# Optimization experiments

Hardware: AMD Instinct MI355X
Metric: run time of the kernel (lower is better)

Reference implementation:

```python
import jax, jax.numpy as jnp
import numpy as np

FEATURE_DIM = 32

def setup_inputs() -> dict:
    key = jax.random.key(0)
    k_pts, k_w1, k_b1, k_w2, k_b2 = jax.random.split(key, 5)
    B, N = 4096, 4096
    points = jax.random.normal(k_pts, (B, N, 2), dtype=jnp.float32)
    # torch Linear default init: U(-1/sqrt(fan_in), 1/sqrt(fan_in))
    lim1 = 1.0 / np.sqrt(10.0)
    lim2 = 1.0 / np.sqrt(64.0)
    W1 = jax.random.uniform(k_w1, (10, 64), minval=-lim1, maxval=lim1, dtype=jnp.float32)
    b1 = jax.random.uniform(k_b1, (64,), minval=-lim1, maxval=lim1, dtype=jnp.float32)
    W2 = jax.random.uniform(k_w2, (64, FEATURE_DIM), minval=-lim2, maxval=lim2, dtype=jnp.float32)
    b2 = jax.random.uniform(k_b2, (FEATURE_DIM,), minval=-lim2, maxval=lim2, dtype=jnp.float32)
    return {"points": points, "W1": W1, "b1": b1, "W2": W2, "b2": b2}

def _geo_features(points):
    # points: (B, N, 2) -> (B, 10)
    bbox_min = jnp.min(points, axis=1)            # (B, 2)
    bbox_max = jnp.max(points, axis=1)            # (B, 2)
    bbox_center = (bbox_min + bbox_max) * 0.5
    bbox_size = bbox_max - bbox_min
    centroid = jnp.mean(points, axis=1)           # (B, 2)
    std = jnp.std(points, axis=1)                 # population std (ddof=0), matches np.std
    diffs = points - centroid[:, None, :]         # (B, N, 2)
    distances = jnp.linalg.norm(diffs, axis=2)    # (B, N)
    dist_mean = jnp.mean(distances, axis=1)       # (B,)
    dist_std = jnp.std(distances, axis=1)         # (B,)
    return jnp.concatenate(
        [bbox_center, bbox_size, centroid, std, dist_mean[:, None], dist_std[:, None]],
        axis=1,
    )  # (B, 10)

def reference(points, W1, b1, W2, b2):
    geo = _geo_features(points)                   # (B, 10)
    h = jax.nn.relu(geo @ W1 + b1)                # (B, 64)
    return jax.nn.relu(h @ W2 + b2)               # (B, feature_dim)
```

## Files before the change

### kernel.cpp

```cpp
#include <hip/hip_runtime.h>
#include <math.h>

#define NPTS 4096
#define BLOCK 256
#define PTS4 (NPTS / 2)
#define ITERS (PTS4 / BLOCK)

__global__ __launch_bounds__(BLOCK, 4) void geo_mlp_kernel(
    const float* __restrict__ points,
    const float* __restrict__ W1,
    const float* __restrict__ b1,
    const float* __restrict__ W2,
    const float* __restrict__ b2,
    float* __restrict__ out)
{
    __shared__ float4 pts[PTS4];
    __shared__ float wred[4][9];
    __shared__ float h[64];

    const int tid  = threadIdx.x;
    const int lane = tid & 63;
    const int wave = tid >> 6;
    const int b    = blockIdx.x;

    float w1r[10];
    float w2r[32];
    float b1r = 0.f, b2r = 0.f;
    const int col   = lane & 31;
    const int rbase = (lane >> 5) * 32;
    if (wave == 0) {
        #pragma unroll
        for (int i = 0; i < 10; ++i)
            w1r[i] = W1[i * 64 + lane];
        b1r = b1[lane];
        #pragma unroll
        for (int r = 0; r < 32; ++r)
            w2r[r] = W2[(rbase + r) * 32 + col];
        b2r = (lane < 32) ? b2[col] : 0.0f;
    }

    const float4* __restrict__ src =
        (const float4*)(points + (size_t)b * NPTS * 2);

    float minx =  INFINITY, miny =  INFINITY;
    float maxx = -INFINITY, maxy = -INFINITY;
    float sx = 0.f, sy = 0.f, sxx = 0.f, syy = 0.f;

    #pragma unroll
    for (int i = 0; i < ITERS; ++i) {
        const int idx = tid + i * BLOCK;
        float4 v = src[idx];
        pts[idx] = v;
        minx = fminf(minx, fminf(v.x, v.z));
        maxx = fmaxf(maxx, fmaxf(v.x, v.z));
        miny = fminf(miny, fminf(v.y, v.w));
        maxy = fmaxf(maxy, fmaxf(v.y, v.w));
        sx += v.x + v.z;
        sy += v.y + v.w;
        sxx = fmaf(v.x, v.x, sxx); sxx = fmaf(v.z, v.z, sxx);
        syy = fmaf(v.y, v.y, syy); syy = fmaf(v.w, v.w, syy);
    }

    #pragma unroll
    for (int off = 32; off > 0; off >>= 1) {
        minx = fminf(minx, __shfl_down(minx, off));
        maxx = fmaxf(maxx, __shfl_down(maxx, off));
        miny = fminf(miny, __shfl_down(miny, off));
        maxy = fmaxf(maxy, __shfl_down(maxy, off));
        sx  += __shfl_down(sx,  off);
        sy  += __shfl_down(sy,  off);
        sxx += __shfl_down(sxx, off);
        syy += __shfl_down(syy, off);
    }
    if (lane == 0) {
        wred[wave][0] = minx; wred[wave][1] = maxx;
        wred[wave][2] = miny; wred[wave][3] = maxy;
        wred[wave][4] = sx;   wred[wave][5] = sy;
        wred[wave][6] = sxx;  wred[wave][7] = syy;
    }
    __syncthreads();

    const float invN = 1.0f / (float)NPTS;
    const float cx = ((wred[0][4] + wred[1][4]) + (wred[2][4] + wred[3][4])) * invN;
    const float cy = ((wred[0][5] + wred[1][5]) + (wred[2][5] + wred[3][5])) * invN;

    float sd = 0.f;
    #pragma unroll
    for (int i = 0; i < ITERS; ++i) {
        float4 v = pts[tid + i * BLOCK];
        float dx0 = v.x - cx, dy0 = v.y - cy;
        float dx1 = v.z - cx, dy1 = v.w - cy;
        sd += sqrtf(fmaf(dx0, dx0, dy0 * dy0));
        sd += sqrtf(fmaf(dx1, dx1, dy1 * dy1));
    }
    #pragma unroll
    for (int off = 32; off > 0; off >>= 1)
        sd += __shfl_down(sd, off);
    if (lane == 0)
        wred[wave][8] = sd;
    __syncthreads();

    if (wave == 0) {
        float fminx = fminf(fminf(wred[0][0], wred[1][0]), fminf(wred[2][0], wred[3][0]));
        float fmaxx = fmaxf(fmaxf(wred[0][1], wred[1][1]), fmaxf(wred[2][1], wred[3][1]));
        float fminy = fminf(fminf(wred[0][2], wred[1][2]), fminf(wred[2][2], wred[3][2]));
        float fmaxy = fmaxf(fmaxf(wred[0][3], wred[1][3]), fmaxf(wred[2][3], wred[3][3]));
        float fsxx = (wred[0][6] + wred[1][6]) + (wred[2][6] + wred[3][6]);
        float fsyy = (wred[0][7] + wred[1][7]) + (wred[2][7] + wred[3][7]);
        float fsd  = (wred[0][8] + wred[1][8]) + (wred[2][8] + wred[3][8]);

        float dist_mean = fsd * invN;
        float ed2 = (fsxx + fsyy) * invN - (cx * cx + cy * cy);
        float dist_std  = sqrtf(fmaxf(ed2 - dist_mean * dist_mean, 0.f));
        float stdx = sqrtf(fmaxf(fsxx * invN - cx * cx, 0.f));
        float stdy = sqrtf(fmaxf(fsyy * invN - cy * cy, 0.f));

        float g[10];
        g[0] = (fminx + fmaxx) * 0.5f;
        g[1] = (fminy + fmaxy) * 0.5f;
        g[2] = fmaxx - fminx;
        g[3] = fmaxy - fminy;
        g[4] = cx;
        g[5] = cy;
        g[6] = stdx;
        g[7] = stdy;
        g[8] = dist_mean;
        g[9] = dist_std;

        float acc = b1r;
        #pragma unroll
        for (int i = 0; i < 10; ++i)
            acc = fmaf(g[i], w1r[i], acc);
        h[lane] = fmaxf(acc, 0.f);

        asm volatile("s_waitcnt lgkmcnt(0)" ::: "memory");

        float acc2 = b2r;
        #pragma unroll
        for (int r = 0; r < 32; ++r)
            acc2 = fmaf(h[rbase + r], w2r[r], acc2);
        acc2 += __shfl_down(acc2, 32);
        if (lane < 32)
            out[(size_t)b * 32 + lane] = fmaxf(acc2, 0.f);
    }
}

extern "C" void kernel_launch(void* const* d_in, const int* in_sizes, int n_in,
                              void* d_out, int out_size, void* d_ws, size_t ws_size,
                              hipStream_t stream) {
    const float* points = (const float*)d_in[0];
    const float* W1     = (const float*)d_in[1];
    const float* b1     = (const float*)d_in[2];
    const float* W2     = (const float*)d_in[3];
    const float* b2     = (const float*)d_in[4];
    float* out          = (float*)d_out;

    const int B = in_sizes[0] / (NPTS * 2);
    geo_mlp_kernel<<<B, BLOCK, 0, stream>>>(points, W1, b1, W2, b2, out);
}
```

Measured before the change: 28.77 us.

## Process eight batches per block with register-prefetched software pipeline

Each block now handles eight batch rows. The next row's global loads are issued into registers while the current row's distance pass and MLP run. This is meant to hide global-load latency and spread the cost of weight loads and launch across rows. In exchange the grid shrinks to B/8 blocks, register pressure rises from the prefetch buffer, and a row count not divisible by eight would be handled incorrectly.

```diff
diff --git a/kernel.cpp b/kernel.cpp
--- a/kernel.cpp
+++ b/kernel.cpp
@@ -5,6 +5,7 @@
 #define BLOCK 256
 #define PTS4 (NPTS / 2)
 #define ITERS (PTS4 / BLOCK)
+#define BPB 8
 
 __global__ __launch_bounds__(BLOCK, 4) void geo_mlp_kernel(
     const float* __restrict__ points,
@@ -15,13 +16,13 @@
     float* __restrict__ out)
 {
     __shared__ float4 pts[PTS4];
-    __shared__ float wred[4][9];
+    __shared__ float wred[2][4][9];
     __shared__ float h[64];
 
     const int tid  = threadIdx.x;
     const int lane = tid & 63;
     const int wave = tid >> 6;
-    const int b    = blockIdx.x;
+    const size_t b0 = (size_t)blockIdx.x * BPB;
 
     float w1r[10];
     float w2r[32];
@@ -39,109 +40,137 @@
         b2r = (lane < 32) ? b2[col] : 0.0f;
     }
 
-    const float4* __restrict__ src =
-        (const float4*)(points + (size_t)b * NPTS * 2);
+    const float invN = 1.0f / (float)NPTS;
+    float4 pn[ITERS];
 
-    float minx =  INFINITY, miny =  INFINITY;
-    float maxx = -INFINITY, maxy = -INFINITY;
-    float sx = 0.f, sy = 0.f, sxx = 0.f, syy = 0.f;
+    auto issue_loads = [&](int j) {
+        const float4* __restrict__ src =
+            (const float4*)(points + (b0 + (size_t)j) * NPTS * 2);
+        #pragma unroll
+        for (int i = 0; i < ITERS; ++i)
+            pn[i] = src[tid + i * BLOCK];
+    };
 
-    #pragma unroll
-    for (int i = 0; i < ITERS; ++i) {
-        const int idx = tid + i * BLOCK;
-        float4 v = src[idx];
-        pts[idx] = v;
-        minx = fminf(minx, fminf(v.x, v.z));
-        maxx = fmaxf(maxx, fmaxf(v.x, v.z));
-        miny = fminf(miny, fminf(v.y, v.w));
-        maxy = fmaxf(maxy, fmaxf(v.y, v.w));
-        sx += v.x + v.z;
-        sy += v.y + v.w;
-        sxx = fmaf(v.x, v.x, sxx); sxx = fmaf(v.z, v.z, sxx);
-        syy = fmaf(v.y, v.y, syy); syy = fmaf(v.w, v.w, syy);
-    }
+    auto stage = [&](int par) {
+        float minx =  INFINITY, miny =  INFINITY;
+        float maxx = -INFINITY, maxy = -INFINITY;
+        float sx = 0.f, sy = 0.f, sxx = 0.f, syy = 0.f;
+        #pragma unroll
+        for (int i = 0; i < ITERS; ++i) {
+            float4 v = pn[i];
+            pts[tid + i * BLOCK] = v;
+            minx = fminf(minx, fminf(v.x, v.z));
+            maxx = fmaxf(maxx, fmaxf(v.x, v.z));
+            miny = fminf(miny, fminf(v.y, v.w));
+            maxy = fmaxf(maxy, fmaxf(v.y, v.w));
+            sx += v.x + v.z;
+            sy += v.y + v.w;
+            sxx = fmaf(v.x, v.x, sxx); sxx = fmaf(v.z, v.z, sxx);
+            syy = fmaf(v.y, v.y, syy); syy = fmaf(v.w, v.w, syy);
+        }
+        #pragma unroll
+        for (int off = 32; off > 0; off >>= 1) {
+            minx = fminf(minx, __shfl_down(minx, off));
+            maxx = fmaxf(maxx, __shfl_down(maxx, off));
+            miny = fminf(miny, __shfl_down(miny, off));
+            maxy = fmaxf(maxy, __shfl_down(maxy, off));
+            sx  += __shfl_down(sx,  off);
+            sy  += __shfl_down(sy,  off);
+            sxx += __shfl_down(sxx, off);
+            syy += __shfl_down(syy, off);
+        }
+        if (lane == 0) {
+            wred[par][wave][0] = minx; wred[par][wave][1] = maxx;
+            wred[par][wave][2] = miny; wred[par][wave][3] = maxy;
+            wred[par][wave][4] = sx;   wred[par][wave][5] = sy;
+            wred[par][wave][6] = sxx;  wred[par][wave][7] = syy;
+        }
+    };
 
-    #pragma unroll
-    for (int off = 32; off > 0; off >>= 1) {
-        minx = fminf(minx, __shfl_down(minx, off));
-        maxx = fmaxf(maxx, __shfl_down(maxx, off));
-        miny = fminf(miny, __shfl_down(miny, off));
-        maxy = fmaxf(maxy, __shfl_down(maxy, off));
-        sx  += __shfl_down(sx,  off);
-        sy  += __shfl_down(sy,  off);
-        sxx += __shfl_down(sxx, off);
-        syy += __shfl_down(syy, off);
-    }
-    if (lane == 0) {
-        wred[wave][0] = minx; wred[wave][1] = maxx;
-        wred[wave][2] = miny; wred[wave][3] = maxy;
-        wred[wave][4] = sx;   wred[wave][5] = sy;
-        wred[wave][6] = sxx;  wred[wave][7] = syy;
-    }
+    issue_loads(0);
+    stage(0);
+    if (BPB > 1) issue_loads(1);
     __syncthreads();
 
-    const float invN = 1.0f / (float)NPTS;
-    const float cx = ((wred[0][4] + wred[1][4]) + (wred[2][4] + wred[3][4])) * invN;
-    const float cy = ((wred[0][5] + wred[1][5]) + (wred[2][5] + wred[3][5])) * invN;
+    for (int j = 0; j < BPB; ++j) {
+        const int par = j & 1;
+        const float cx = ((wred[par][0][4] + wred[par][1][4]) +
+                          (wred[par][2][4] + wred[par][3][4])) * invN;
+        const float cy = ((wred[par][0][5] + wred[par][1][5]) +
+                          (wred[par][2][5] + wred[par][3][5])) * invN;
 
-    float sd = 0.f;
-    #pragma unroll
-    for (int i = 0; i < ITERS; ++i) {
-        float4 v = pts[tid + i * BLOCK];
-        float dx0 = v.x - cx, dy0 = v.y - cy;
-        float dx1 = v.z - cx, dy1 = v.w - cy;
-        sd += sqrtf(fmaf(dx0, dx0, dy0 * dy0));
-        sd += sqrtf(fmaf(dx1, dx1, dy1 * dy1));
-    }
-    #pragma unroll
-    for (int off = 32; off > 0; off >>= 1)
-        sd += __shfl_down(sd, off);
-    if (lane == 0)
-        wred[wave][8] = sd;
-    __syncthreads();
+        float sd = 0.f;
+        #pragma unroll
+        for (int i = 0; i < ITERS; ++i) {
+            float4 v = pts[tid + i * BLOCK];
+            float dx0 = v.x - cx, dy0 = v.y - cy;
+            float dx1 = v.z - cx, dy1 = v.w - cy;
+            sd += sqrtf(fmaf(dx0, dx0, dy0 * dy0));
+            sd += sqrtf(fmaf(dx1, dx1, dy1 * dy1));
+        }
+        #pragma unroll
+        for (int off = 32; off > 0; off >>= 1)
+            sd += __shfl_down(sd, off);
+        if (lane == 0)
+            wred[par][wave][8] = sd;
+        __syncthreads();
 
-    if (wave == 0) {
-        float fminx = fminf(fminf(wred[0][0], wred[1][0]), fminf(wred[2][0], wred[3][0]));
-        float fmaxx = fmaxf(fmaxf(wred[0][1], wred[1][1]), fmaxf(wred[2][1], wred[3][1]));
-        float fminy = fminf(fminf(wred[0][2], wred[1][2]), fminf(wred[2][2], wred[3][2]));
-        float fmaxy = fmaxf(fmaxf(wred[0][3], wred[1][3]), fmaxf(wred[2][3], wred[3][3]));
-        float fsxx = (wred[0][6] + wred[1][6]) + (wred[2][6] + wred[3][6]);
-        float fsyy = (wred[0][7] + wred[1][7]) + (wred[2][7] + wred[3][7]);
-        float fsd  = (wred[0][8] + wred[1][8]) + (wred[2][8] + wred[3][8]);
+        if (j + 1 < BPB) {
+            stage((j + 1) & 1);
+            if (j + 2 < BPB) issue_loads(j + 2);
+        }
 
-        float dist_mean = fsd * invN;
-        float ed2 = (fsxx + fsyy) * invN - (cx * cx + cy * cy);
-        float dist_std  = sqrtf(fmaxf(ed2 - dist_mean * dist_mean, 0.f));
-        float stdx = sqrtf(fmaxf(fsxx * invN - cx * cx, 0.f));
-        float stdy = sqrtf(fmaxf(fsyy * invN - cy * cy, 0.f));
+        if (wave == 0) {
+            float fminx = fminf(fminf(wred[par][0][0], wred[par][1][0]),
+                                fminf(wred[par][2][0], wred[par][3][0]));
+            float fmaxx = fmaxf(fmaxf(wred[par][0][1], wred[par][1][1]),
+                                fmaxf(wred[par][2][1], wred[par][3][1]));
+            float fminy = fminf(fminf(wred[par][0][2], wred[par][1][2]),
+                                fminf(wred[par][2][2], wred[par][3][2]));
+            float fmaxy = fmaxf(fmaxf(wred[par][0][3], wred[par][1][3]),
+                                fmaxf(wred[par][2][3], wred[par][3][3]));
+            float fsxx = (wred[par][0][6] + wred[par][1][6]) +
+                         (wred[par][2][6] + wred[par][3][6]);
+            float fsyy = (wred[par][0][7] + wred[par][1][7]) +
+                         (wred[par][2][7] + wred[par][3][7]);
+            float fsd  = (wred[par][0][8] + wred[par][1][8]) +
+                         (wred[par][2][8] + wred[par][3][8]);
 
-        float g[10];
-        g[0] = (fminx + fmaxx) * 0.5f;
-        g[1] = (fminy + fmaxy) * 0.5f;
-        g[2] = fmaxx - fminx;
-        g[3] = fmaxy - fminy;
-        g[4] = cx;
-        g[5] = cy;
-        g[6] = stdx;
-        g[7] = stdy;
-        g[8] = dist_mean;
-        g[9] = dist_std;
+            float dist_mean = fsd * invN;
+            float ed2 = (fsxx + fsyy) * invN - (cx * cx + cy * cy);
+            float dist_std = sqrtf(fmaxf(ed2 - dist_mean * dist_mean, 0.f));
+            float stdx = sqrtf(fmaxf(fsxx * invN - cx * cx, 0.f));
+            float stdy = sqrtf(fmaxf(fsyy * invN - cy * cy, 0.f));
 
-        float acc = b1r;
-        #pragma unroll
-        for (int i = 0; i < 10; ++i)
-            acc = fmaf(g[i], w1r[i], acc);
-        h[lane] = fmaxf(acc, 0.f);
+            float g[10];
+            g[0] = (fminx + fmaxx) * 0.5f;
+            g[1] = (fminy + fmaxy) * 0.5f;
+            g[2] = fmaxx - fminx;
+            g[3] = fmaxy - fminy;
+            g[4] = cx;
+            g[5] = cy;
+            g[6] = stdx;
+            g[7] = stdy;
+            g[8] = dist_mean;
+            g[9] = dist_std;
 
-        asm volatile("s_waitcnt lgkmcnt(0)" ::: "memory");
+            float acc = b1r;
+            #pragma unroll
+            for (int i = 0; i < 10; ++i)
+                acc = fmaf(g[i], w1r[i], acc);
+            h[lane] = fmaxf(acc, 0.f);
 
-        float acc2 = b2r;
-        #pragma unroll
-        for (int r = 0; r < 32; ++r)
-            acc2 = fmaf(h[rbase + r], w2r[r], acc2);
-        acc2 += __shfl_down(acc2, 32);
-        if (lane < 32)
-            out[(size_t)b * 32 + lane] = fmaxf(acc2, 0.f);
+            asm volatile("s_waitcnt lgkmcnt(0)" ::: "memory");
+
+            float acc2 = b2r;
+            #pragma unroll
+            for (int r = 0; r < 32; ++r)
+                acc2 = fmaf(h[rbase + r], w2r[r], acc2);
+            acc2 += __shfl_down(acc2, 32);
+            if (lane < 32)
+                out[(b0 + (size_t)j) * 32 + lane] = fmaxf(acc2, 0.f);
+        }
+        __syncthreads();
     }
 }
 
@@ -156,5 +185,5 @@
     float* out          = (float*)d_out;
 
     const int B = in_sizes[0] / (NPTS * 2);
-    geo_mlp_kernel<<<B, BLOCK, 0, stream>>>(points, W1, b1, W2, b2, out);
+    geo_mlp_kernel<<<B / BPB, BLOCK, 0, stream>>>(points, W1, b1, W2, b2, out);
 }
```

New measurement: 39.65 us. 1.38x slower.

## Process each batch row with a single wavefront holding points in registers

Applied to the files above, without the earlier changes.

Switches from a 256-thread block per row with shared-memory staging to one 64-lane wave per row, keeping all points in registers across both passes. Removes the shared-memory buffer, the block barriers and the cross-wave reductions, and computes the second MLP layer with lane shuffles instead of LDS. The cost is heavy VGPR use (about 128 registers for points), which lowers occupancy, and every wave now loads its own copy of the weights.

```diff
diff --git a/kernel.cpp b/kernel.cpp
--- a/kernel.cpp
+++ b/kernel.cpp
@@ -2,11 +2,10 @@
 #include <math.h>
 
 #define NPTS 4096
-#define BLOCK 256
 #define PTS4 (NPTS / 2)
-#define ITERS (PTS4 / BLOCK)
+#define LPL  (PTS4 / 64)
 
-__global__ __launch_bounds__(BLOCK, 4) void geo_mlp_kernel(
+__global__ __launch_bounds__(64, 2) void geo_mlp_kernel(
     const float* __restrict__ points,
     const float* __restrict__ W1,
     const float* __restrict__ b1,
@@ -14,43 +13,35 @@
     const float* __restrict__ b2,
     float* __restrict__ out)
 {
-    __shared__ float4 pts[PTS4];
-    __shared__ float wred[4][9];
-    __shared__ float h[64];
+    const int lane  = threadIdx.x;
+    const size_t b  = blockIdx.x;
 
-    const int tid  = threadIdx.x;
-    const int lane = tid & 63;
-    const int wave = tid >> 6;
-    const int b    = blockIdx.x;
+    const float4* __restrict__ src =
+        (const float4*)(points + b * (size_t)(NPTS * 2));
 
-    float w1r[10];
-    float w2r[32];
-    float b1r = 0.f, b2r = 0.f;
+    float4 pn[LPL];
+    #pragma unroll
+    for (int i = 0; i < LPL; ++i)
+        pn[i] = src[lane + i * 64];
+
     const int col   = lane & 31;
     const int rbase = (lane >> 5) * 32;
-    if (wave == 0) {
-        #pragma unroll
-        for (int i = 0; i < 10; ++i)
-            w1r[i] = W1[i * 64 + lane];
-        b1r = b1[lane];
-        #pragma unroll
-        for (int r = 0; r < 32; ++r)
-            w2r[r] = W2[(rbase + r) * 32 + col];
-        b2r = (lane < 32) ? b2[col] : 0.0f;
-    }
-
-    const float4* __restrict__ src =
-        (const float4*)(points + (size_t)b * NPTS * 2);
+    float w1r[10], w2r[32];
+    #pragma unroll
+    for (int i = 0; i < 10; ++i)
+        w1r[i] = W1[i * 64 + lane];
+    float b1r = b1[lane];
+    #pragma unroll
+    for (int r = 0; r < 32; ++r)
+        w2r[r] = W2[(rbase + r) * 32 + col];
+    float b2r = (lane < 32) ? b2[col] : 0.0f;
 
     float minx =  INFINITY, miny =  INFINITY;
     float maxx = -INFINITY, maxy = -INFINITY;
     float sx = 0.f, sy = 0.f, sxx = 0.f, syy = 0.f;
-
     #pragma unroll
-    for (int i = 0; i < ITERS; ++i) {
-        const int idx = tid + i * BLOCK;
-        float4 v = src[idx];
-        pts[idx] = v;
+    for (int i = 0; i < LPL; ++i) {
+        float4 v = pn[i];
         minx = fminf(minx, fminf(v.x, v.z));
         maxx = fmaxf(maxx, fmaxf(v.x, v.z));
         miny = fminf(miny, fminf(v.y, v.w));
@@ -62,87 +53,65 @@
     }
 
     #pragma unroll
-    for (int off = 32; off > 0; off >>= 1) {
-        minx = fminf(minx, __shfl_down(minx, off));
-        maxx = fmaxf(maxx, __shfl_down(maxx, off));
-        miny = fminf(miny, __shfl_down(miny, off));
-        maxy = fmaxf(maxy, __shfl_down(maxy, off));
-        sx  += __shfl_down(sx,  off);
-        sy  += __shfl_down(sy,  off);
-        sxx += __shfl_down(sxx, off);
-        syy += __shfl_down(syy, off);
+    for (int m = 32; m > 0; m >>= 1) {
+        minx = fminf(minx, __shfl_xor(minx, m));
+        maxx = fmaxf(maxx, __shfl_xor(maxx, m));
+        miny = fminf(miny, __shfl_xor(miny, m));
+        maxy = fmaxf(maxy, __shfl_xor(maxy, m));
+        sx  += __shfl_xor(sx,  m);
+        sy  += __shfl_xor(sy,  m);
+        sxx += __shfl_xor(sxx, m);
+        syy += __shfl_xor(syy, m);
     }
-    if (lane == 0) {
-        wred[wave][0] = minx; wred[wave][1] = maxx;
-        wred[wave][2] = miny; wred[wave][3] = maxy;
-        wred[wave][4] = sx;   wred[wave][5] = sy;
-        wred[wave][6] = sxx;  wred[wave][7] = syy;
-    }
-    __syncthreads();
 
     const float invN = 1.0f / (float)NPTS;
-    const float cx = ((wred[0][4] + wred[1][4]) + (wred[2][4] + wred[3][4])) * invN;
-    const float cy = ((wred[0][5] + wred[1][5]) + (wred[2][5] + wred[3][5])) * invN;
+    const float cx = sx * invN;
+    const float cy = sy * invN;
 
     float sd = 0.f;
     #pragma unroll
-    for (int i = 0; i < ITERS; ++i) {
-        float4 v = pts[tid + i * BLOCK];
+    for (int i = 0; i < LPL; ++i) {
+        float4 v = pn[i];
         float dx0 = v.x - cx, dy0 = v.y - cy;
         float dx1 = v.z - cx, dy1 = v.w - cy;
         sd += sqrtf(fmaf(dx0, dx0, dy0 * dy0));
         sd += sqrtf(fmaf(dx1, dx1, dy1 * dy1));
     }
     #pragma unroll
-    for (int off = 32; off > 0; off >>= 1)
-        sd += __shfl_down(sd, off);
-    if (lane == 0)
-        wred[wave][8] = sd;
-    __syncthreads();
+    for (int m = 32; m > 0; m >>= 1)
+        sd += __shfl_xor(sd, m);
 
-    if (wave == 0) {
-        float fminx = fminf(fminf(wred[0][0], wred[1][0]), fminf(wred[2][0], wred[3][0]));
-        float fmaxx = fmaxf(fmaxf(wred[0][1], wred[1][1]), fmaxf(wred[2][1], wred[3][1]));
-        float fminy = fminf(fminf(wred[0][2], wred[1][2]), fminf(wred[2][2], wred[3][2]));
-        float fmaxy = fmaxf(fmaxf(wred[0][3], wred[1][3]), fmaxf(wred[2][3], wred[3][3]));
-        float fsxx = (wred[0][6] + wred[1][6]) + (wred[2][6] + wred[3][6]);
-        float fsyy = (wred[0][7] + wred[1][7]) + (wred[2][7] + wred[3][7]);
-        float fsd  = (wred[0][8] + wred[1][8]) + (wred[2][8] + wred[3][8]);
+    float dist_mean = sd * invN;
+    float ed2 = (sxx + syy) * invN - (cx * cx + cy * cy);
+    float dist_std = sqrtf(fmaxf(ed2 - dist_mean * dist_mean, 0.f));
+    float stdx = sqrtf(fmaxf(sxx * invN - cx * cx, 0.f));
+    float stdy = sqrtf(fmaxf(syy * invN - cy * cy, 0.f));
 
-        float dist_mean = fsd * invN;
-        float ed2 = (fsxx + fsyy) * invN - (cx * cx + cy * cy);
-        float dist_std  = sqrtf(fmaxf(ed2 - dist_mean * dist_mean, 0.f));
-        float stdx = sqrtf(fmaxf(fsxx * invN - cx * cx, 0.f));
-        float stdy = sqrtf(fmaxf(fsyy * invN - cy * cy, 0.f));
+    float g[10];
+    g[0] = (minx + maxx) * 0.5f;
+    g[1] = (miny + maxy) * 0.5f;
+    g[2] = maxx - minx;
+    g[3] = maxy - miny;
+    g[4] = cx;
+    g[5] = cy;
+    g[6] = stdx;
+    g[7] = stdy;
+    g[8] = dist_mean;
+    g[9] = dist_std;
 
-        float g[10];
-        g[0] = (fminx + fmaxx) * 0.5f;
-        g[1] = (fminy + fmaxy) * 0.5f;
-        g[2] = fmaxx - fminx;
-        g[3] = fmaxy - fminy;
-        g[4] = cx;
-        g[5] = cy;
-        g[6] = stdx;
-        g[7] = stdy;
-        g[8] = dist_mean;
-        g[9] = dist_std;
+    float hval = b1r;
+    #pragma unroll
+    for (int i = 0; i < 10; ++i)
+        hval = fmaf(g[i], w1r[i], hval);
+    hval = fmaxf(hval, 0.f);
 
-        float acc = b1r;
-        #pragma unroll
-        for (int i = 0; i < 10; ++i)
-            acc = fmaf(g[i], w1r[i], acc);
-        h[lane] = fmaxf(acc, 0.f);
-
-        asm volatile("s_waitcnt lgkmcnt(0)" ::: "memory");
-
-        float acc2 = b2r;
-        #pragma unroll
-        for (int r = 0; r < 32; ++r)
-            acc2 = fmaf(h[rbase + r], w2r[r], acc2);
-        acc2 += __shfl_down(acc2, 32);
-        if (lane < 32)
-            out[(size_t)b * 32 + lane] = fmaxf(acc2, 0.f);
-    }
+    float acc2 = b2r;
+    #pragma unroll
+    for (int r = 0; r < 32; ++r)
+        acc2 = fmaf(__shfl(hval, rbase + r), w2r[r], acc2);
+    acc2 += __shfl_down(acc2, 32);
+    if (lane < 32)
+        out[b * 32 + lane] = fmaxf(acc2, 0.f);
 }
 
 extern "C" void kernel_launch(void* const* d_in, const int* in_sizes, int n_in,
@@ -156,5 +125,5 @@
     float* out          = (float*)d_out;
 
     const int B = in_sizes[0] / (NPTS * 2);
-    geo_mlp_kernel<<<B, BLOCK, 0, stream>>>(points, W1, b1, W2, b2, out);
+    geo_mlp_kernel<<<B, 64, 0, stream>>>(points, W1, b1, W2, b2, out);
 }
```

Measured after the change: 30.31 us. +5.3%, slower.
